# Kernel optimization log

Hardware: AMD Instinct MI355X
Metric: run time of the kernel (lower is better)

Reference implementation:

```python
import jax, jax.numpy as jnp
import numpy as np

B, N, D, A, E, T, H, O = 2, 2048, 64, 16, 2, 5, 128, 1


def setup_inputs() -> dict:
    key = jax.random.key(0)
    ks = jax.random.split(key, 12)
    s = 0.02  # torch init: normal(0, 0.02), biases zero
    return {
        "prop_state": jax.random.normal(ks[0], (B, N, D), jnp.float32),
        "annotation": jax.random.normal(ks[1], (B, N, A), jnp.float32),
        "adj_mat": jax.random.uniform(ks[2], (B, N, 2 * N * E), jnp.float32),
        "W_in": s * jax.random.normal(ks[3], (E, D, D), jnp.float32),
        "b_in": jnp.zeros((E, D), jnp.float32),
        "W_out": s * jax.random.normal(ks[4], (E, D, D), jnp.float32),
        "b_out": jnp.zeros((E, D), jnp.float32),
        "Wr": s * jax.random.normal(ks[5], (3 * D, D), jnp.float32),
        "br": jnp.zeros((D,), jnp.float32),
        "Wz": s * jax.random.normal(ks[6], (3 * D, D), jnp.float32),
        "bz": jnp.zeros((D,), jnp.float32),
        "Wh": s * jax.random.normal(ks[7], (3 * D, D), jnp.float32),
        "bh": jnp.zeros((D,), jnp.float32),
        "Wo1": s * jax.random.normal(ks[8], (D + A, H), jnp.float32),
        "bo1": jnp.zeros((H,), jnp.float32),
        "Wo2": s * jax.random.normal(ks[9], (H, O), jnp.float32),
        "bo2": jnp.zeros((O,), jnp.float32),
    }


def reference(prop_state, annotation, adj_mat, W_in, b_in, W_out, b_out,
              Wr, br, Wz, bz, Wh, bh, Wo1, bo1, Wo2, bo2):
    Bb, Nn, Dd = prop_state.shape
    Ee = W_in.shape[0]
    A_in = adj_mat[:, :, : Nn * Ee]   # [B, N, E*N]
    A_out = adj_mat[:, :, Nn * Ee :]  # [B, N, E*N]
    h = prop_state
    for _ in range(T):
        # per-edge-type linear maps; edge-type-major flatten (index = e*N + v)
        ins = (jnp.einsum('bnd,edk->benk', h, W_in) + b_in[None, :, None, :]).reshape(Bb, Ee * Nn, Dd)
        outs = (jnp.einsum('bnd,edk->benk', h, W_out) + b_out[None, :, None, :]).reshape(Bb, Ee * Nn, Dd)
        a_in = jnp.einsum('bnm,bmd->bnd', A_in, ins)
        a_out = jnp.einsum('bnm,bmd->bnd', A_out, outs)
        a = jnp.concatenate([a_in, a_out, h], axis=-1)          # [B, N, 3D]
        r = jax.nn.sigmoid(a @ Wr + br)
        z = jax.nn.sigmoid(a @ Wz + bz)
        joint = jnp.concatenate([a_in, a_out, r * h], axis=-1)  # [B, N, 3D]
        h_hat = jnp.tanh(joint @ Wh + bh)
        h = (1.0 - z) * h + z * h_hat
    x = jnp.concatenate([h, annotation], axis=-1)               # [B, N, D+A]
    x = jax.nn.sigmoid(x @ Wo1 + bo1)
    x = x @ Wo2 + bo2                                           # [B, N, O]
    return x.sum(axis=2)                                        # [B, N]
```

## Files before the change

### kernel.cpp

```cpp
#include <hip/hip_runtime.h>
#include <cstdint>
#include <cstddef>

#define B_ 2
#define N_ 2048
#define D_ 64
#define E_ 2
#define T_ 5

typedef short bf16x8 __attribute__((ext_vector_type(8)));
typedef unsigned short u16x8 __attribute__((ext_vector_type(8)));
typedef float f32x16 __attribute__((ext_vector_type(16)));

__device__ __forceinline__ unsigned short f2bf(float f) {
    unsigned int x = __float_as_uint(f);
    x += 0x7FFFu + ((x >> 16) & 1u);
    return (unsigned short)(x >> 16);
}

__global__ void convert_kernel(const float* __restrict__ adj, u16x8* __restrict__ Abf) {
    int rt = blockIdx.x, c = blockIdx.y, bd = blockIdx.z;
    int b = bd >> 1, dir = bd & 1;
    int tid = threadIdx.x;

    __shared__ __align__(16) unsigned short sb[32][520];

    const float* base = adj + ((size_t)(b * N_ + rt * 32)) * (2 * N_ * E_) + dir * (N_ * E_) + c * 512;

    #pragma unroll
    for (int p = 0; p < 4; ++p) {
        int r = p * 8 + (tid >> 5);
        int i = tid & 31;
        const float* rowp = base + (size_t)r * (2 * N_ * E_);
        #pragma unroll
        for (int j = 0; j < 4; ++j) {
            float4 f = *(const float4*)(rowp + i * 4 + j * 128);
            int kl = i * 4 + j * 128;
            sb[r][kl + 0] = f2bf(f.x);
            sb[r][kl + 1] = f2bf(f.y);
            sb[r][kl + 2] = f2bf(f.z);
            sb[r][kl + 3] = f2bf(f.w);
        }
    }
    __syncthreads();

    int l = tid & 63;
    int row = l & 31, khalf = l >> 5;
    int ktl0 = tid >> 6;
    u16x8* dst = Abf + ((size_t)(bd * 64 + rt) * 256 + c * 32 + ktl0) * 64 + l;
    #pragma unroll
    for (int q = 0; q < 8; ++q) {
        int ktl = ktl0 + q * 4;
        u16x8 v = *(const u16x8*)&sb[row][ktl * 16 + khalf * 8];
        dst[(size_t)q * 4 * 64] = v;
    }
}

__global__ void transform0_kernel(const float* __restrict__ h,
                                  const float* __restrict__ W_in, const float* __restrict__ b_in,
                                  const float* __restrict__ W_out, const float* __restrict__ b_out,
                                  u16x8* __restrict__ VT) {
    int y = blockIdx.y;
    int e = y & 1, dir = (y >> 1) & 1, b = y >> 2;
    int bd = y >> 1;
    const float* W = (dir ? W_out : W_in) + e * D_ * D_;
    const float* bias = (dir ? b_out : b_in) + e * D_;
    int n0 = blockIdx.x * 64;

    __shared__ float hs[64][65];
    __shared__ float Ws[64][64];
    __shared__ float os[64][65];

    int tid = threadIdx.x;
    #pragma unroll
    for (int i = 0; i < 16; ++i) {
        int idx = tid + 256 * i;
        int r = idx >> 6, c = idx & 63;
        hs[r][c] = h[((size_t)(b * N_ + n0 + r)) * D_ + c];
        Ws[r][c] = W[idx];
    }
    __syncthreads();

    int g = tid >> 6, l = tid & 63;
    float acc[16];
    #pragma unroll
    for (int j = 0; j < 16; ++j) acc[j] = bias[g * 16 + j];
    for (int k = 0; k < 64; ++k) {
        float hv = hs[l][k];
        #pragma unroll
        for (int j = 0; j < 16; ++j) acc[j] = fmaf(hv, Ws[k][g * 16 + j], acc[j]);
    }
    #pragma unroll
    for (int j = 0; j < 16; ++j) os[l][g * 16 + j] = acc[j];
    __syncthreads();

    #pragma unroll
    for (int c = 0; c < 2; ++c) {
        int chunk = tid + 256 * c;
        int kt_local = chunk >> 7;
        int sub = (chunk >> 6) & 1;
        int ln = chunk & 63;
        int d = sub * 32 + (ln & 31);
        int nbase = kt_local * 16 + (ln >> 5) * 8;
        u16x8 o;
        #pragma unroll
        for (int j = 0; j < 8; ++j) o[j] = f2bf(os[nbase + j][d]);
        int ktg = e * 128 + blockIdx.x * 4 + kt_local;
        VT[((size_t)bd * 512 + ktg * 2 + sub) * 64 + ln] = o;
    }
}

__global__ void __launch_bounds__(512, 2) aggregate_kernel(
        const bf16x8* __restrict__ Abf, const bf16x8* __restrict__ VT,
        float* __restrict__ apart) {
    int bx = blockIdx.x;
    int bd = blockIdx.y;
    int sp = blockIdx.z;
    int tid = threadIdx.x;
    int w = tid >> 6, lane = tid & 63;
    int rt = bx * 8 + w;
    int kt0 = sp * 32;

    const bf16x8* Ap = Abf + ((size_t)(bd * 64 + rt) * 256 + kt0) * 64 + lane;
    const bf16x8* Vp = VT + (size_t)bd * 32768 + (size_t)kt0 * 128 + lane;

    f32x16 acc0 = {}, acc1 = {};
    #pragma unroll 4
    for (int kk = 0; kk < 32; ++kk) {
        bf16x8 a  = Ap[(size_t)kk * 64];
        bf16x8 b0 = Vp[(size_t)kk * 128];
        bf16x8 b1 = Vp[(size_t)kk * 128 + 64];
        acc0 = __builtin_amdgcn_mfma_f32_32x32x16_bf16(a, b0, acc0, 0, 0, 0);
        acc1 = __builtin_amdgcn_mfma_f32_32x32x16_bf16(a, b1, acc1, 0, 0, 0);
    }

    float* Cp = apart + ((size_t)(sp * 4 + bd) * 2048) * 64;
    int col = lane & 31;
    int rbase = rt * 32 + 4 * (lane >> 5);
    #pragma unroll
    for (int reg = 0; reg < 16; ++reg) {
        int row = rbase + (reg & 3) + 8 * (reg >> 2);
        Cp[(size_t)row * 64 + col]      = acc0[reg];
        Cp[(size_t)row * 64 + col + 32] = acc1[reg];
    }
}

__device__ __forceinline__ void gru_core(
        const float* __restrict__ h_in, const float* __restrict__ apart,
        const float* __restrict__ Wr, const float* __restrict__ br,
        const float* __restrict__ Wz, const float* __restrict__ bz,
        const float* __restrict__ Wh, const float* __restrict__ bh,
        float sa[16][3][64], float hs[16][64],
        int b, int n0, int g0, int tid)
{
    int nl = tid >> 6, d = tid & 63;
    int n = n0 + nl;
    float ain = 0.f, aout = 0.f;
    #pragma unroll
    for (int sp = 0; sp < 8; ++sp) {
        ain  += apart[(((size_t)(sp * 4 + b * 2    )) * 2048 + n) * 64 + d];
        aout += apart[(((size_t)(sp * 4 + b * 2 + 1)) * 2048 + n) * 64 + d];
    }
    float h_d = h_in[((size_t)g0 + nl) * 64 + d];
    sa[nl][0][d] = ain;
    sa[nl][1][d] = aout;
    sa[nl][2][d] = h_d;
    float accr = br[d], accz = bz[d];
    #pragma unroll 8
    for (int k = 0; k < 64; ++k) {
        float a0 = sa[nl][0][k], a1 = sa[nl][1][k], a2 = sa[nl][2][k];
        accr = fmaf(a0, Wr[k * 64 + d], accr);
        accr = fmaf(a1, Wr[(64 + k) * 64 + d], accr);
        accr = fmaf(a2, Wr[(128 + k) * 64 + d], accr);
        accz = fmaf(a0, Wz[k * 64 + d], accz);
        accz = fmaf(a1, Wz[(64 + k) * 64 + d], accz);
        accz = fmaf(a2, Wz[(128 + k) * 64 + d], accz);
    }
    float r = 1.0f / (1.0f + expf(-accr));
    float z = 1.0f / (1.0f + expf(-accz));
    sa[nl][2][d] = r * h_d;
    float acch = bh[d];
    #pragma unroll 8
    for (int k = 0; k < 64; ++k) {
        float a0 = sa[nl][0][k], a1 = sa[nl][1][k], a2 = sa[nl][2][k];
        acch = fmaf(a0, Wh[k * 64 + d], acch);
        acch = fmaf(a1, Wh[(64 + k) * 64 + d], acch);
        acch = fmaf(a2, Wh[(128 + k) * 64 + d], acch);
    }
    float hh = tanhf(acch);
    hs[nl][d] = (1.0f - z) * h_d + z * hh;
}

__global__ void __launch_bounds__(1024, 1) gru_mid_kernel(
        const float* __restrict__ h_in, float* __restrict__ h_out,
        const float* __restrict__ apart,
        const float* __restrict__ Wr, const float* __restrict__ br,
        const float* __restrict__ Wz, const float* __restrict__ bz,
        const float* __restrict__ Wh, const float* __restrict__ bh,
        const float* __restrict__ W_in, const float* __restrict__ b_in,
        const float* __restrict__ W_out, const float* __restrict__ b_out,
        u16x8* __restrict__ VT)
{
    __shared__ float sa[16][3][64];
    __shared__ float hs[16][64];
    __shared__ float os[4][16][66];

    int wg = blockIdx.x, tid = threadIdx.x;
    int g0 = wg * 16;
    int b = g0 >> 11, n0 = g0 & 2047;
    int ktgl = n0 >> 4;

    gru_core(h_in, apart, Wr, br, Wz, bz, Wh, bh, sa, hs, b, n0, g0, tid);

    {
        int nl = tid >> 6, d = tid & 63;
        h_out[((size_t)g0 + nl) * 64 + d] = hs[nl][d];
    }
    __syncthreads();

    int u = tid >> 6, lane = tid & 63;
    {
        int de = u & 3, q = u >> 2;
        int dir = de >> 1, e = de & 1;
        const float* W    = (dir ? W_out : W_in) + e * D_ * D_;
        const float* bias = (dir ? b_out : b_in) + e * D_;
        int d = lane;
        float acc[4];
        #pragma unroll
        for (int i = 0; i < 4; ++i) acc[i] = bias[d];
        for (int k = 0; k < 64; ++k) {
            float wv = W[k * 64 + d];
            #pragma unroll
            for (int i = 0; i < 4; ++i) acc[i] = fmaf(hs[q * 4 + i][k], wv, acc[i]);
        }
        #pragma unroll
        for (int i = 0; i < 4; ++i) os[de][q * 4 + i][d] = acc[i];
    }
    __syncthreads();

    if (u < 8) {
        int de = u >> 1, sub = u & 1;
        int dir = de >> 1, e = de & 1;
        int dd = sub * 32 + (lane & 31);
        int nb = (lane >> 5) * 8;
        u16x8 o;
        #pragma unroll
        for (int j = 0; j < 8; ++j) o[j] = f2bf(os[de][nb + j][dd]);
        int bd = b * 2 + dir;
        int ktg = e * 128 + ktgl;
        VT[((size_t)bd * 512 + ktg * 2 + sub) * 64 + lane] = o;
    }
}

__global__ void __launch_bounds__(1024, 1) gru_last_kernel(
        const float* __restrict__ h_in,
        const float* __restrict__ apart,
        const float* __restrict__ Wr, const float* __restrict__ br,
        const float* __restrict__ Wz, const float* __restrict__ bz,
        const float* __restrict__ Wh, const float* __restrict__ bh,
        const float* __restrict__ ann,
        const float* __restrict__ Wo1, const float* __restrict__ bo1,
        const float* __restrict__ Wo2, const float* __restrict__ bo2,
        float* __restrict__ out)
{
    __shared__ float sa[16][3][64];
    __shared__ float hs[16][64];
    __shared__ float red[8][2][2];

    int wg = blockIdx.x, tid = threadIdx.x;
    int g0 = wg * 16;
    int b = g0 >> 11, n0 = g0 & 2047;

    gru_core(h_in, apart, Wr, br, Wz, bz, Wh, bh, sa, hs, b, n0, g0, tid);
    __syncthreads();

    int sub = tid >> 7, j = tid & 127;
    int wv = (tid >> 6) & 1;
    #pragma unroll
    for (int s = 0; s < 2; ++s) {
        int nl = sub * 2 + s;
        int g = g0 + nl;
        float acc = bo1[j];
        #pragma unroll
        for (int i = 0; i < 64; ++i) acc = fmaf(hs[nl][i], Wo1[i * 128 + j], acc);
        #pragma unroll
        for (int i = 0; i < 16; ++i) acc = fmaf(ann[(size_t)g * 16 + i], Wo1[(64 + i) * 128 + j], acc);
        float y = 1.0f / (1.0f + expf(-acc));
        float v = y * Wo2[j];
        #pragma unroll
        for (int off = 32; off > 0; off >>= 1) v += __shfl_down(v, off, 64);
        if ((tid & 63) == 0) red[sub][wv][s] = v;
    }
    __syncthreads();
    if (j == 0) {
        #pragma unroll
        for (int s = 0; s < 2; ++s)
            out[g0 + sub * 2 + s] = red[sub][0][s] + red[sub][1][s] + bo2[0];
    }
}

extern "C" void kernel_launch(void* const* d_in, const int* in_sizes, int n_in,
                              void* d_out, int out_size, void* d_ws, size_t ws_size,
                              hipStream_t stream) {
    const float* prop = (const float*)d_in[0];
    const float* ann  = (const float*)d_in[1];
    const float* adj  = (const float*)d_in[2];
    const float* W_in = (const float*)d_in[3];
    const float* b_in = (const float*)d_in[4];
    const float* W_out= (const float*)d_in[5];
    const float* b_out= (const float*)d_in[6];
    const float* Wr   = (const float*)d_in[7];
    const float* br   = (const float*)d_in[8];
    const float* Wz   = (const float*)d_in[9];
    const float* bz   = (const float*)d_in[10];
    const float* Wh   = (const float*)d_in[11];
    const float* bh   = (const float*)d_in[12];
    const float* Wo1  = (const float*)d_in[13];
    const float* bo1  = (const float*)d_in[14];
    const float* Wo2  = (const float*)d_in[15];
    const float* bo2  = (const float*)d_in[16];
    float* out = (float*)d_out;

    char* ws = (char*)d_ws;
    u16x8* Abf    = (u16x8*)ws;
    u16x8* VT     = (u16x8*)(ws + (64ull << 20));
    float* apart  = (float*)(ws + (66ull << 20));
    float* h      = (float*)(ws + (82ull << 20));

    convert_kernel<<<dim3(64, 8, 4), 256, 0, stream>>>(adj, Abf);
    transform0_kernel<<<dim3(32, 8), 256, 0, stream>>>(
        prop, W_in, b_in, W_out, b_out, VT);

    for (int t = 0; t < T_; ++t) {
        aggregate_kernel<<<dim3(8, 4, 8), 512, 0, stream>>>(
            (const bf16x8*)Abf, (const bf16x8*)VT, apart);
        const float* h_in = (t == 0) ? prop : h;
        if (t < T_ - 1) {
            gru_mid_kernel<<<dim3(256), 1024, 0, stream>>>(
                h_in, h, apart, Wr, br, Wz, bz, Wh, bh,
                W_in, b_in, W_out, b_out, VT);
        } else {
            gru_last_kernel<<<dim3(256), 1024, 0, stream>>>(
                h_in, apart, Wr, br, Wz, bz, Wh, bh,
                ann, Wo1, bo1, Wo2, bo2, out);
        }
    }
}
```

Baseline: 490.7 us.

## Merge prep kernels and split aggregate K dimension across more blocks

Fuses the adjacency bf16 conversion and the initial transform into one launch by dispatching on block index with a shared-memory union, removing one kernel launch. The aggregate kernel now uses 256-thread blocks with a 16-way K split instead of 8-way, giving 1024 blocks instead of 256 for more parallelism on the GPU. The GRU step must now reduce twice as many partial sums from a larger apart buffer, so the workspace layout for h is moved to make room.

```diff
diff --git a/kernel.cpp b/kernel.cpp
--- a/kernel.cpp
+++ b/kernel.cpp
@@ -7,6 +7,7 @@
 #define D_ 64
 #define E_ 2
 #define T_ 5
+#define NSPLIT 16
 
 typedef short bf16x8 __attribute__((ext_vector_type(8)));
 typedef unsigned short u16x8 __attribute__((ext_vector_type(8)));
@@ -18,99 +19,99 @@
     return (unsigned short)(x >> 16);
 }
 
-__global__ void convert_kernel(const float* __restrict__ adj, u16x8* __restrict__ Abf) {
-    int rt = blockIdx.x, c = blockIdx.y, bd = blockIdx.z;
-    int b = bd >> 1, dir = bd & 1;
+struct ConvSM { unsigned short sb[32][520]; };
+struct TranSM { float hs[64][65]; float Ws[64][64]; float os[64][65]; };
+
+__global__ void prep_kernel(const float* __restrict__ adj, u16x8* __restrict__ Abf,
+                            const float* __restrict__ prop,
+                            const float* __restrict__ W_in, const float* __restrict__ b_in,
+                            const float* __restrict__ W_out, const float* __restrict__ b_out,
+                            u16x8* __restrict__ VT) {
+    __shared__ union { ConvSM c; TranSM t; } sm;
     int tid = threadIdx.x;
 
-    __shared__ __align__(16) unsigned short sb[32][520];
-
-    const float* base = adj + ((size_t)(b * N_ + rt * 32)) * (2 * N_ * E_) + dir * (N_ * E_) + c * 512;
-
-    #pragma unroll
-    for (int p = 0; p < 4; ++p) {
-        int r = p * 8 + (tid >> 5);
-        int i = tid & 31;
-        const float* rowp = base + (size_t)r * (2 * N_ * E_);
-        #pragma unroll
-        for (int j = 0; j < 4; ++j) {
-            float4 f = *(const float4*)(rowp + i * 4 + j * 128);
-            int kl = i * 4 + j * 128;
-            sb[r][kl + 0] = f2bf(f.x);
-            sb[r][kl + 1] = f2bf(f.y);
-            sb[r][kl + 2] = f2bf(f.z);
-            sb[r][kl + 3] = f2bf(f.w);
-        }
-    }
-    __syncthreads();
-
-    int l = tid & 63;
-    int row = l & 31, khalf = l >> 5;
-    int ktl0 = tid >> 6;
-    u16x8* dst = Abf + ((size_t)(bd * 64 + rt) * 256 + c * 32 + ktl0) * 64 + l;
-    #pragma unroll
-    for (int q = 0; q < 8; ++q) {
-        int ktl = ktl0 + q * 4;
-        u16x8 v = *(const u16x8*)&sb[row][ktl * 16 + khalf * 8];
-        dst[(size_t)q * 4 * 64] = v;
-    }
-}
-
-__global__ void transform0_kernel(const float* __restrict__ h,
-                                  const float* __restrict__ W_in, const float* __restrict__ b_in,
-                                  const float* __restrict__ W_out, const float* __restrict__ b_out,
-                                  u16x8* __restrict__ VT) {
-    int y = blockIdx.y;
-    int e = y & 1, dir = (y >> 1) & 1, b = y >> 2;
-    int bd = y >> 1;
-    const float* W = (dir ? W_out : W_in) + e * D_ * D_;
-    const float* bias = (dir ? b_out : b_in) + e * D_;
-    int n0 = blockIdx.x * 64;
-
-    __shared__ float hs[64][65];
-    __shared__ float Ws[64][64];
-    __shared__ float os[64][65];
-
-    int tid = threadIdx.x;
-    #pragma unroll
-    for (int i = 0; i < 16; ++i) {
-        int idx = tid + 256 * i;
-        int r = idx >> 6, c = idx & 63;
-        hs[r][c] = h[((size_t)(b * N_ + n0 + r)) * D_ + c];
-        Ws[r][c] = W[idx];
-    }
-    __syncthreads();
-
-    int g = tid >> 6, l = tid & 63;
-    float acc[16];
-    #pragma unroll
-    for (int j = 0; j < 16; ++j) acc[j] = bias[g * 16 + j];
-    for (int k = 0; k < 64; ++k) {
-        float hv = hs[l][k];
-        #pragma unroll
-        for (int j = 0; j < 16; ++j) acc[j] = fmaf(hv, Ws[k][g * 16 + j], acc[j]);
-    }
-    #pragma unroll
-    for (int j = 0; j < 16; ++j) os[l][g * 16 + j] = acc[j];
-    __syncthreads();
-
-    #pragma unroll
-    for (int c = 0; c < 2; ++c) {
-        int chunk = tid + 256 * c;
-        int kt_local = chunk >> 7;
-        int sub = (chunk >> 6) & 1;
-        int ln = chunk & 63;
-        int d = sub * 32 + (ln & 31);
-        int nbase = kt_local * 16 + (ln >> 5) * 8;
-        u16x8 o;
-        #pragma unroll
-        for (int j = 0; j < 8; ++j) o[j] = f2bf(os[nbase + j][d]);
-        int ktg = e * 128 + blockIdx.x * 4 + kt_local;
-        VT[((size_t)bd * 512 + ktg * 2 + sub) * 64 + ln] = o;
-    }
-}
-
-__global__ void __launch_bounds__(512, 2) aggregate_kernel(
+    if (blockIdx.x < 2048) {
+        int idx = blockIdx.x;
+        int rt = idx & 63, c = (idx >> 6) & 7, bd = idx >> 9;
+        int b = bd >> 1, dir = bd & 1;
+        const float* base = adj + ((size_t)(b * N_ + rt * 32)) * (2 * N_ * E_) + dir * (N_ * E_) + c * 512;
+
+        #pragma unroll
+        for (int p = 0; p < 4; ++p) {
+            int r = p * 8 + (tid >> 5);
+            int i = tid & 31;
+            const float* rowp = base + (size_t)r * (2 * N_ * E_);
+            #pragma unroll
+            for (int j = 0; j < 4; ++j) {
+                float4 f = *(const float4*)(rowp + i * 4 + j * 128);
+                int kl = i * 4 + j * 128;
+                sm.c.sb[r][kl + 0] = f2bf(f.x);
+                sm.c.sb[r][kl + 1] = f2bf(f.y);
+                sm.c.sb[r][kl + 2] = f2bf(f.z);
+                sm.c.sb[r][kl + 3] = f2bf(f.w);
+            }
+        }
+        __syncthreads();
+
+        int l = tid & 63;
+        int row = l & 31, khalf = l >> 5;
+        int ktl0 = tid >> 6;
+        u16x8* dst = Abf + ((size_t)(bd * 64 + rt) * 256 + c * 32 + ktl0) * 64 + l;
+        #pragma unroll
+        for (int q = 0; q < 8; ++q) {
+            int ktl = ktl0 + q * 4;
+            u16x8 v = *(const u16x8*)&sm.c.sb[row][ktl * 16 + khalf * 8];
+            dst[(size_t)q * 4 * 64] = v;
+        }
+    } else {
+        int idx = blockIdx.x - 2048;
+        int bx = idx & 31, y = idx >> 5;
+        int e = y & 1, dir = (y >> 1) & 1, b = y >> 2;
+        int bd = y >> 1;
+        const float* W = (dir ? W_out : W_in) + e * D_ * D_;
+        const float* bias = (dir ? b_out : b_in) + e * D_;
+        int n0 = bx * 64;
+
+        #pragma unroll
+        for (int i = 0; i < 16; ++i) {
+            int ii = tid + 256 * i;
+            int r = ii >> 6, c = ii & 63;
+            sm.t.hs[r][c] = prop[((size_t)(b * N_ + n0 + r)) * D_ + c];
+            sm.t.Ws[r][c] = W[ii];
+        }
+        __syncthreads();
+
+        int g = tid >> 6, l = tid & 63;
+        float acc[16];
+        #pragma unroll
+        for (int j = 0; j < 16; ++j) acc[j] = bias[g * 16 + j];
+        for (int k = 0; k < 64; ++k) {
+            float hv = sm.t.hs[l][k];
+            #pragma unroll
+            for (int j = 0; j < 16; ++j) acc[j] = fmaf(hv, sm.t.Ws[k][g * 16 + j], acc[j]);
+        }
+        #pragma unroll
+        for (int j = 0; j < 16; ++j) sm.t.os[l][g * 16 + j] = acc[j];
+        __syncthreads();
+
+        #pragma unroll
+        for (int c = 0; c < 2; ++c) {
+            int chunk = tid + 256 * c;
+            int kt_local = chunk >> 7;
+            int sub = (chunk >> 6) & 1;
+            int ln = chunk & 63;
+            int d = sub * 32 + (ln & 31);
+            int nbase = kt_local * 16 + (ln >> 5) * 8;
+            u16x8 o;
+            #pragma unroll
+            for (int j = 0; j < 8; ++j) o[j] = f2bf(sm.t.os[nbase + j][d]);
+            int ktg = e * 128 + bx * 4 + kt_local;
+            VT[((size_t)bd * 512 + ktg * 2 + sub) * 64 + ln] = o;
+        }
+    }
+}
+
+__global__ void __launch_bounds__(256, 4) aggregate_kernel(
         const bf16x8* __restrict__ Abf, const bf16x8* __restrict__ VT,
         float* __restrict__ apart) {
     int bx = blockIdx.x;
@@ -118,15 +119,15 @@
     int sp = blockIdx.z;
     int tid = threadIdx.x;
     int w = tid >> 6, lane = tid & 63;
-    int rt = bx * 8 + w;
-    int kt0 = sp * 32;
+    int rt = bx * 4 + w;
+    int kt0 = sp * 16;
 
     const bf16x8* Ap = Abf + ((size_t)(bd * 64 + rt) * 256 + kt0) * 64 + lane;
     const bf16x8* Vp = VT + (size_t)bd * 32768 + (size_t)kt0 * 128 + lane;
 
     f32x16 acc0 = {}, acc1 = {};
     #pragma unroll 4
-    for (int kk = 0; kk < 32; ++kk) {
+    for (int kk = 0; kk < 16; ++kk) {
         bf16x8 a  = Ap[(size_t)kk * 64];
         bf16x8 b0 = Vp[(size_t)kk * 128];
         bf16x8 b1 = Vp[(size_t)kk * 128 + 64];
@@ -157,7 +158,7 @@
     int n = n0 + nl;
     float ain = 0.f, aout = 0.f;
     #pragma unroll
-    for (int sp = 0; sp < 8; ++sp) {
+    for (int sp = 0; sp < NSPLIT; ++sp) {
         ain  += apart[(((size_t)(sp * 4 + b * 2    )) * 2048 + n) * 64 + d];
         aout += apart[(((size_t)(sp * 4 + b * 2 + 1)) * 2048 + n) * 64 + d];
     }
@@ -325,14 +326,13 @@
     u16x8* Abf    = (u16x8*)ws;
     u16x8* VT     = (u16x8*)(ws + (64ull << 20));
     float* apart  = (float*)(ws + (66ull << 20));
-    float* h      = (float*)(ws + (82ull << 20));
-
-    convert_kernel<<<dim3(64, 8, 4), 256, 0, stream>>>(adj, Abf);
-    transform0_kernel<<<dim3(32, 8), 256, 0, stream>>>(
-        prop, W_in, b_in, W_out, b_out, VT);
+    float* h      = (float*)(ws + (100ull << 20));
+
+    prep_kernel<<<dim3(2048 + 256), 256, 0, stream>>>(
+        adj, Abf, prop, W_in, b_in, W_out, b_out, VT);
 
     for (int t = 0; t < T_; ++t) {
-        aggregate_kernel<<<dim3(8, 4, 8), 512, 0, stream>>>(
+        aggregate_kernel<<<dim3(16, 4, NSPLIT), 256, 0, stream>>>(
             (const bf16x8*)Abf, (const bf16x8*)VT, apart);
         const float* h_in = (t == 0) ? prop : h;
         if (t < T_ - 1) {
```

New measurement: 507.2 us. 3.4% more time.
